# Kernel optimization log

Hardware: AMD Instinct MI355X
Metric: run time of the kernel (lower is better)

Reference implementation:

```python
import jax, jax.numpy as jnp
import numpy as np

SCALE = 1.0 / 8.0  # source divides sim_M by literal 8 (== sqrt(d_k=64))


def setup_inputs() -> dict:
    key = jax.random.key(0)
    ks = jax.random.split(key, 7)
    B, S, D = 16, 2048, 512  # D = n_head * d_k = 8 * 64
    s = 1.0 / np.sqrt(D)
    return {
        "x": jax.random.normal(ks[0], (B, S, D), dtype=jnp.float32),
        "Wq": jax.random.normal(ks[1], (D, D), dtype=jnp.float32) * s,
        "bq": jax.random.normal(ks[2], (D,), dtype=jnp.float32) * 0.01,
        "Wk": jax.random.normal(ks[3], (D, D), dtype=jnp.float32) * s,
        "bk": jax.random.normal(ks[4], (D,), dtype=jnp.float32) * 0.01,
        "Wv": jax.random.normal(ks[5], (D, D), dtype=jnp.float32) * s,
        "bv": jax.random.normal(ks[6], (D,), dtype=jnp.float32) * 0.01,
    }


def reference(x, Wq, bq, Wk, bk, Wv, bv):
    # Manual QKV projections (no head split, matching the source code)
    q = jnp.einsum("bsd,de->bse", x, Wq) + bq  # [B,S,D]
    k = jnp.einsum("bsd,de->bse", x, Wk) + bk  # [B,S,D]
    v = jnp.einsum("bsd,de->bse", x, Wv) + bv  # [B,S,D]
    # bmm -> softmax -> bmm attention
    sim = jnp.einsum("bqe,bke->bqk", q, k) * SCALE  # [B,S,S]
    attn = jax.nn.softmax(sim, axis=-1)
    out = jnp.einsum("bqk,bkd->bqd", attn, v)  # [B,S,D]
    return out
```

## Files before the change

kernel.cpp:

```cpp
#include <hip/hip_runtime.h>
#include <math.h>

typedef _Float16 f16;
typedef _Float16 f16x2 __attribute__((ext_vector_type(2)));
typedef _Float16 f16x8 __attribute__((ext_vector_type(8)));
typedef float f32x4 __attribute__((ext_vector_type(4)));

#define NB 16
#define SS 2048
#define DD 512

__device__ __forceinline__ void gl_lds16(const void* g, void* l) {
  __builtin_amdgcn_global_load_lds(
      (const __attribute__((address_space(1))) unsigned int*)g,
      (__attribute__((address_space(3))) unsigned int*)l, 16, 0, 0);
}

__device__ __forceinline__ int pk2(float a, float b) {
  f16x2 t = {(f16)a, (f16)b};
  return __builtin_bit_cast(int, t);
}

__global__ __launch_bounds__(256) void cast_kernel(const float* __restrict__ x,
                                                   f16* __restrict__ o) {
  size_t i = (size_t)blockIdx.x * 256 + threadIdx.x;
  const float4* p = (const float4*)x + i * 2;
  float4 a = p[0], b = p[1];
  f16x8 v = {(f16)a.x, (f16)a.y, (f16)a.z, (f16)a.w,
             (f16)b.x, (f16)b.y, (f16)b.z, (f16)b.w};
  *((f16x8*)o + i) = v;
}

__global__ __launch_bounds__(256) void transpose_kernel(
    const float* __restrict__ W0, const float* __restrict__ W1,
    const float* __restrict__ W2, f16* __restrict__ T0, f16* __restrict__ T1,
    f16* __restrict__ T2) {
  const float* W = (blockIdx.z == 0) ? W0 : (blockIdx.z == 1) ? W1 : W2;
  f16* Wt = (blockIdx.z == 0) ? T0 : (blockIdx.z == 1) ? T1 : T2;
  __shared__ float t[32][33];
  int bx = blockIdx.x * 32, by = blockIdx.y * 32;
  int c = threadIdx.x & 31, r0 = threadIdx.x >> 5;
  for (int r = r0; r < 32; r += 8) t[r][c] = W[(size_t)(by + r) * DD + bx + c];
  __syncthreads();
  for (int r = r0; r < 32; r += 8) Wt[(size_t)(bx + r) * DD + by + c] = (f16)t[c][r];
}

__global__ __launch_bounds__(512, 2) void gemmQKV_kernel(
    const f16* __restrict__ xh, const f16* __restrict__ WqT,
    const f16* __restrict__ WkT, const f16* __restrict__ WvT,
    f16* __restrict__ Qh, f16* __restrict__ Kh, f16* __restrict__ Vth,
    const float* __restrict__ bq, const float* __restrict__ bk,
    const float* __restrict__ bv) {
  const int wid = (blockIdx.x & 7) * 96 + (blockIdx.x >> 3);
  const f16* Wm;
  f16* C;
  const float* bias;
  size_t x0;
  size_t crow0, ccol0;
  int w0, ldc, bias_row;
  float scale;
  bool isV;
  if (wid < 512) {
    const bool isK = wid >= 256;
    const int r = wid & 255;
    x0 = (size_t)(r >> 1) * 256;
    w0 = (r & 1) * 256;
    Wm = isK ? WkT : WqT;
    C = isK ? Kh : Qh;
    bias = isK ? bk : bq;
    crow0 = x0;
    ccol0 = (size_t)w0;
    ldc = DD;
    bias_row = 0;
    scale = isK ? 1.0f : 0.125f;
    isV = false;
  } else {
    const int v = wid - 512;
    const int b = v >> 4, e = (v >> 3) & 1, s = v & 7;
    x0 = (size_t)b * SS + (size_t)s * 256;
    w0 = e * 256;
    Wm = WvT;
    C = Vth + (size_t)b * DD * SS;
    bias = bv;
    crow0 = (size_t)w0;
    ccol0 = (size_t)s * 256;
    ldc = SS;
    bias_row = 1;
    scale = 1.0f;
    isV = true;
  }
  __shared__ f16 Xsh[2][256][64];
  __shared__ f16 Wsh[2][256][64];
  const int tid = threadIdx.x, lane = tid & 63, wave = tid >> 6;
  const int wm2 = wave >> 2, wn2 = wave & 3;
  const int l15 = lane & 15, lq = lane >> 4;
  const int srow = lane >> 3;
  const int sseg = (lane & 7) ^ srow;
  f32x4 acc[8][4] = {};
  auto stage = [&](int sb, int kt) {
#pragma unroll
    for (int g = 0; g < 4; ++g) {
      const int r0 = wave * 32 + g * 8;
      gl_lds16(xh + (x0 + r0 + srow) * DD + kt * 64 + sseg * 8,
               (f16*)&Xsh[sb][r0][0] + lane * 8);
      gl_lds16(Wm + (size_t)(w0 + r0 + srow) * DD + kt * 64 + sseg * 8,
               (f16*)&Wsh[sb][r0][0] + lane * 8);
    }
  };
  stage(0, 0);
  asm volatile("s_waitcnt vmcnt(0)" ::: "memory");
  asm volatile("s_barrier" ::: "memory");
  for (int kt = 0; kt < 8; ++kt) {
    const int buf = kt & 1;
    if (kt < 7) stage(buf ^ 1, kt + 1);
    const f16(*As)[64] = isV ? Wsh[buf] : Xsh[buf];
    const f16(*Bs)[64] = isV ? Xsh[buf] : Wsh[buf];
#pragma unroll
    for (int ks = 0; ks < 2; ++ks) {
      const int seg = ((ks * 4 + lq) ^ (l15 & 7)) * 8;
      f16x8 bf[4];
#pragma unroll
      for (int j = 0; j < 4; ++j)
        bf[j] = *(const f16x8*)&Bs[64 * wn2 + 16 * j + l15][seg];
#pragma unroll
      for (int mh = 0; mh < 2; ++mh) {
        f16x8 af[4];
#pragma unroll
        for (int i = 0; i < 4; ++i)
          af[i] = *(const f16x8*)&As[128 * wm2 + 64 * mh + 16 * i + l15][seg];
        __builtin_amdgcn_s_setprio(1);
#pragma unroll
        for (int i = 0; i < 4; ++i)
#pragma unroll
          for (int j = 0; j < 4; ++j)
            acc[4 * mh + i][j] = __builtin_amdgcn_mfma_f32_16x16x32_f16(
                af[i], bf[j], acc[4 * mh + i][j], 0, 0, 0);
        __builtin_amdgcn_s_setprio(0);
        if (ks == 1 && mh == 1)
          asm volatile("s_waitcnt vmcnt(0)" ::: "memory");
        asm volatile("s_barrier" ::: "memory");
      }
    }
  }
#pragma unroll
  for (int i = 0; i < 8; ++i) {
    const int arow = 128 * wm2 + 16 * i + 4 * lq;
#pragma unroll
    for (int j = 0; j < 4; ++j) {
      const int acol = 64 * wn2 + 16 * j + l15;
#pragma unroll
      for (int r = 0; r < 4; ++r) {
        const size_t rr = crow0 + arow + r;
        const size_t cc = ccol0 + acol;
        const float bvv = bias_row ? bias[rr] : bias[cc];
        C[rr * ldc + cc] = (f16)((acc[i][j][r] + bvv) * scale);
      }
    }
  }
}

__global__ __launch_bounds__(512, 2) void attn_kernel(
    const f16* __restrict__ Q, const f16* __restrict__ K,
    const f16* __restrict__ Vt, float* __restrict__ out) {
  const int id = blockIdx.x;
  const int b = (id & 7) + ((id >> 7) << 3);
  const int qt = (id >> 3) & 15;
  const int tid = threadIdx.x, lane = tid & 63, wave = tid >> 6;
  const int l15 = lane & 15, lq = lane >> 4;

  __shared__ __align__(16) f16 Kl[2][32][520];
  __shared__ __align__(16) f16 Vl[2][512][32];

  const f16* qp = Q + ((size_t)(b * SS + qt * 128 + wave * 16 + l15)) * DD + lq * 8;
  f16x8 qf[16];
#pragma unroll
  for (int kk = 0; kk < 16; ++kk) qf[kk] = *(const f16x8*)(qp + kk * 32);

  const f16* Kb = K + (size_t)b * SS * DD;
  const f16* Vb = Vt + (size_t)b * DD * SS;

  const int sdata = (lane & 3) ^ ((lane >> 3) & 3);
  const int vrow = lane >> 2;
  const int vs_off = (lq ^ ((l15 >> 1) & 3)) * 8;

  f16x8 onef;
#pragma unroll
  for (int j = 0; j < 8; ++j) onef[j] = (f16)1.0f;

  auto stage = [&](int sb, int kb) {
#pragma unroll
    for (int rr = 0; rr < 4; ++rr) {
      int row = wave * 4 + rr;
      gl_lds16(Kb + ((size_t)(kb + row)) * DD + lane * 8, &Kl[sb][row][lane * 8]);
    }
#pragma unroll
    for (int i = 0; i < 4; ++i) {
      int e0 = wave * 64 + i * 16;
      gl_lds16(Vb + (size_t)(e0 + vrow) * SS + kb + sdata * 8,
               (f16*)&Vl[sb][e0][0] + lane * 8);
    }
  };

  stage(0, 0);
  __syncthreads();

  f32x4 acco[32] = {};
  f32x4 accl = {};
  float m = -1e30f;

  for (int it = 0; it < 64; ++it) {
    const int buf = it & 1;
    if (it < 63) stage(buf ^ 1, (it + 1) * 32);
    f32x4 sa0 = {}, sa1 = {};
#pragma unroll
    for (int kk = 0; kk < 16; ++kk) {
      f16x8 b0 = *(const f16x8*)&Kl[buf][l15][kk * 32 + lq * 8];
      f16x8 b1 = *(const f16x8*)&Kl[buf][16 + l15][kk * 32 + lq * 8];
      sa0 = __builtin_amdgcn_mfma_f32_16x16x32_f16(b0, qf[kk], sa0, 0, 0, 0);
      sa1 = __builtin_amdgcn_mfma_f32_16x16x32_f16(b1, qf[kk], sa1, 0, 0, 0);
    }
    float lm = fmaxf(fmaxf(fmaxf(sa0[0], sa0[1]), fmaxf(sa0[2], sa0[3])),
                     fmaxf(fmaxf(sa1[0], sa1[1]), fmaxf(sa1[2], sa1[3])));
    if (__any(lm > m + 8.0f)) {
      float mx = lm;
      mx = fmaxf(mx, __shfl_xor(mx, 16));
      mx = fmaxf(mx, __shfl_xor(mx, 32));
      float mn = fmaxf(m, mx);
      float al = __expf(m - mn);
      m = mn;
      float alr[4];
#pragma unroll
      for (int r = 0; r < 4; ++r) alr[r] = __shfl(al, 4 * lq + r);
#pragma unroll
      for (int t = 0; t < 32; ++t)
#pragma unroll
        for (int r = 0; r < 4; ++r) acco[t][r] *= alr[r];
#pragma unroll
      for (int r = 0; r < 4; ++r) accl[r] *= alr[r];
    }
    int A0 = pk2(__expf(sa0[0] - m), __expf(sa0[1] - m));
    int A1 = pk2(__expf(sa0[2] - m), __expf(sa0[3] - m));
    int B0 = pk2(__expf(sa1[0] - m), __expf(sa1[1] - m));
    int B1 = pk2(__expf(sa1[2] - m), __expf(sa1[3] - m));
    const bool low = (lq < 2);
    int s0 = low ? B0 : A0, s1 = low ? B1 : A1;
    int X0 = __shfl_xor(s0, 32), X1 = __shfl_xor(s1, 32);
    int Y0 = low ? A0 : B0, Y1 = low ? A1 : B1;
    const bool sx = (lq == 0) || (lq == 3);
    int t0 = sx ? X0 : Y0, t1 = sx ? X1 : Y1;
    int Z0 = __shfl_xor(t0, 16), Z1 = __shfl_xor(t1, 16);
    union PU { int i[4]; f16x8 v; } pu;
    pu.i[0] = (lq == 0) ? Y0 : ((lq == 2) ? X0 : Z0);
    pu.i[1] = (lq == 0) ? Y1 : ((lq == 2) ? X1 : Z1);
    pu.i[2] = (lq == 1) ? X0 : ((lq == 3) ? Y0 : Z0);
    pu.i[3] = (lq == 1) ? X1 : ((lq == 3) ? Y1 : Z1);
    f16x8 pa = pu.v;
    accl = __builtin_amdgcn_mfma_f32_16x16x32_f16(pa, onef, accl, 0, 0, 0);
#pragma unroll
    for (int nn = 0; nn < 32; ++nn) {
      f16x8 vf = *(const f16x8*)&Vl[buf][nn * 16 + l15][vs_off];
      acco[nn] = __builtin_amdgcn_mfma_f32_16x16x32_f16(pa, vf, acco[nn], 0, 0, 0);
    }
    __syncthreads();
  }
  float inv[4];
#pragma unroll
  for (int r = 0; r < 4; ++r) inv[r] = 1.0f / accl[r];
  const size_t ob = ((size_t)(b * SS + qt * 128 + wave * 16 + 4 * lq)) * DD + l15;
#pragma unroll
  for (int nn = 0; nn < 32; ++nn)
#pragma unroll
    for (int r = 0; r < 4; ++r)
      out[ob + (size_t)r * DD + nn * 16] = acco[nn][r] * inv[r];
}

extern "C" void kernel_launch(void* const* d_in, const int* in_sizes, int n_in,
                              void* d_out, int out_size, void* d_ws, size_t ws_size,
                              hipStream_t stream) {
  const float* x = (const float*)d_in[0];
  const float* Wq = (const float*)d_in[1];
  const float* bq = (const float*)d_in[2];
  const float* Wk = (const float*)d_in[3];
  const float* bk = (const float*)d_in[4];
  const float* Wv = (const float*)d_in[5];
  const float* bv = (const float*)d_in[6];
  float* out = (float*)d_out;
  f16* ws = (f16*)d_ws;
  const size_t NX = (size_t)NB * SS * DD;
  f16* xh = ws;
  f16* Qh = ws + NX;
  f16* Kh = ws + 2 * NX;
  f16* Vth = ws + 3 * NX;
  f16* WqT = ws + 4 * NX;
  f16* WkT = WqT + DD * DD;
  f16* WvT = WkT + DD * DD;

  cast_kernel<<<NX / 8 / 256, 256, 0, stream>>>(x, xh);
  transpose_kernel<<<dim3(16, 16, 3), 256, 0, stream>>>(Wq, Wk, Wv, WqT, WkT, WvT);
  gemmQKV_kernel<<<768, 512, 0, stream>>>(xh, WqT, WkT, WvT, Qh, Kh, Vth, bq, bk, bv);
  attn_kernel<<<256, 512, 0, stream>>>(Qh, Kh, Vth, out);
}
```

Baseline: 365.1 us.

## Process two 16-row query tiles per wave in attention, halving waves per block

Each wave in the attention kernel now handles 32 query rows (two 16-row tiles) instead of 16, with 4 waves per block instead of 8. Each K and V fragment read from LDS is reused across two MFMA chains, which halves LDS read traffic per flop. In exchange every wave holds twice the accumulators and Q fragments, which raises register pressure (launch bounds become 256,1). It also leaves fewer waves per CU to hide latency.

```diff
diff --git a/kernel.cpp b/kernel.cpp
--- a/kernel.cpp
+++ b/kernel.cpp
@@ -159,7 +159,7 @@
   }
 }
 
-__global__ __launch_bounds__(512, 2) void attn_kernel(
+__global__ __launch_bounds__(256, 1) void attn_kernel(
     const f16* __restrict__ Q, const f16* __restrict__ K,
     const f16* __restrict__ Vt, float* __restrict__ out) {
   const int id = blockIdx.x;
@@ -171,10 +171,12 @@
   __shared__ __align__(16) f16 Kl[2][32][520];
   __shared__ __align__(16) f16 Vl[2][512][32];
 
-  const f16* qp = Q + ((size_t)(b * SS + qt * 128 + wave * 16 + l15)) * DD + lq * 8;
-  f16x8 qf[16];
-#pragma unroll
-  for (int kk = 0; kk < 16; ++kk) qf[kk] = *(const f16x8*)(qp + kk * 32);
+  const f16* qp0 = Q + ((size_t)(b * SS + qt * 128 + wave * 32 + l15)) * DD + lq * 8;
+  f16x8 qf0[16], qf1[16];
+#pragma unroll
+  for (int kk = 0; kk < 16; ++kk) qf0[kk] = *(const f16x8*)(qp0 + kk * 32);
+#pragma unroll
+  for (int kk = 0; kk < 16; ++kk) qf1[kk] = *(const f16x8*)(qp0 + 16 * DD + kk * 32);
 
   const f16* Kb = K + (size_t)b * SS * DD;
   const f16* Vb = Vt + (size_t)b * DD * SS;
@@ -189,13 +191,13 @@
 
   auto stage = [&](int sb, int kb) {
 #pragma unroll
-    for (int rr = 0; rr < 4; ++rr) {
-      int row = wave * 4 + rr;
+    for (int rr = 0; rr < 8; ++rr) {
+      int row = wave * 8 + rr;
       gl_lds16(Kb + ((size_t)(kb + row)) * DD + lane * 8, &Kl[sb][row][lane * 8]);
     }
 #pragma unroll
-    for (int i = 0; i < 4; ++i) {
-      int e0 = wave * 64 + i * 16;
+    for (int i = 0; i < 8; ++i) {
+      int e0 = wave * 128 + i * 16;
       gl_lds16(Vb + (size_t)(e0 + vrow) * SS + kb + sdata * 8,
                (f16*)&Vl[sb][e0][0] + lane * 8);
     }
@@ -204,74 +206,90 @@
   stage(0, 0);
   __syncthreads();
 
-  f32x4 acco[32] = {};
-  f32x4 accl = {};
-  float m = -1e30f;
+  f32x4 acco0[32] = {}, acco1[32] = {};
+  f32x4 accl0 = {}, accl1 = {};
+  float m0 = -1e30f, m1 = -1e30f;
 
   for (int it = 0; it < 64; ++it) {
     const int buf = it & 1;
     if (it < 63) stage(buf ^ 1, (it + 1) * 32);
-    f32x4 sa0 = {}, sa1 = {};
+    f32x4 s00 = {}, s01 = {}, s10 = {}, s11 = {};
 #pragma unroll
     for (int kk = 0; kk < 16; ++kk) {
       f16x8 b0 = *(const f16x8*)&Kl[buf][l15][kk * 32 + lq * 8];
       f16x8 b1 = *(const f16x8*)&Kl[buf][16 + l15][kk * 32 + lq * 8];
-      sa0 = __builtin_amdgcn_mfma_f32_16x16x32_f16(b0, qf[kk], sa0, 0, 0, 0);
-      sa1 = __builtin_amdgcn_mfma_f32_16x16x32_f16(b1, qf[kk], sa1, 0, 0, 0);
-    }
-    float lm = fmaxf(fmaxf(fmaxf(sa0[0], sa0[1]), fmaxf(sa0[2], sa0[3])),
-                     fmaxf(fmaxf(sa1[0], sa1[1]), fmaxf(sa1[2], sa1[3])));
-    if (__any(lm > m + 8.0f)) {
-      float mx = lm;
-      mx = fmaxf(mx, __shfl_xor(mx, 16));
-      mx = fmaxf(mx, __shfl_xor(mx, 32));
-      float mn = fmaxf(m, mx);
-      float al = __expf(m - mn);
-      m = mn;
-      float alr[4];
-#pragma unroll
-      for (int r = 0; r < 4; ++r) alr[r] = __shfl(al, 4 * lq + r);
-#pragma unroll
-      for (int t = 0; t < 32; ++t)
-#pragma unroll
-        for (int r = 0; r < 4; ++r) acco[t][r] *= alr[r];
-#pragma unroll
-      for (int r = 0; r < 4; ++r) accl[r] *= alr[r];
-    }
-    int A0 = pk2(__expf(sa0[0] - m), __expf(sa0[1] - m));
-    int A1 = pk2(__expf(sa0[2] - m), __expf(sa0[3] - m));
-    int B0 = pk2(__expf(sa1[0] - m), __expf(sa1[1] - m));
-    int B1 = pk2(__expf(sa1[2] - m), __expf(sa1[3] - m));
-    const bool low = (lq < 2);
-    int s0 = low ? B0 : A0, s1 = low ? B1 : A1;
-    int X0 = __shfl_xor(s0, 32), X1 = __shfl_xor(s1, 32);
-    int Y0 = low ? A0 : B0, Y1 = low ? A1 : B1;
-    const bool sx = (lq == 0) || (lq == 3);
-    int t0 = sx ? X0 : Y0, t1 = sx ? X1 : Y1;
-    int Z0 = __shfl_xor(t0, 16), Z1 = __shfl_xor(t1, 16);
-    union PU { int i[4]; f16x8 v; } pu;
-    pu.i[0] = (lq == 0) ? Y0 : ((lq == 2) ? X0 : Z0);
-    pu.i[1] = (lq == 0) ? Y1 : ((lq == 2) ? X1 : Z1);
-    pu.i[2] = (lq == 1) ? X0 : ((lq == 3) ? Y0 : Z0);
-    pu.i[3] = (lq == 1) ? X1 : ((lq == 3) ? Y1 : Z1);
-    f16x8 pa = pu.v;
-    accl = __builtin_amdgcn_mfma_f32_16x16x32_f16(pa, onef, accl, 0, 0, 0);
+      s00 = __builtin_amdgcn_mfma_f32_16x16x32_f16(b0, qf0[kk], s00, 0, 0, 0);
+      s01 = __builtin_amdgcn_mfma_f32_16x16x32_f16(b1, qf0[kk], s01, 0, 0, 0);
+      s10 = __builtin_amdgcn_mfma_f32_16x16x32_f16(b0, qf1[kk], s10, 0, 0, 0);
+      s11 = __builtin_amdgcn_mfma_f32_16x16x32_f16(b1, qf1[kk], s11, 0, 0, 0);
+    }
+    f16x8 pa0, pa1;
+#pragma unroll
+    for (int h = 0; h < 2; ++h) {
+      f32x4 sa0 = h ? s10 : s00;
+      f32x4 sa1 = h ? s11 : s01;
+      float& m = h ? m1 : m0;
+      f32x4& accl = h ? accl1 : accl0;
+      f32x4* acco = h ? acco1 : acco0;
+      float lm = fmaxf(fmaxf(fmaxf(sa0[0], sa0[1]), fmaxf(sa0[2], sa0[3])),
+                       fmaxf(fmaxf(sa1[0], sa1[1]), fmaxf(sa1[2], sa1[3])));
+      if (__any(lm > m + 8.0f)) {
+        float mx = fmaxf(lm, __shfl_xor(lm, 16));
+        mx = fmaxf(mx, __shfl_xor(mx, 32));
+        float mn = fmaxf(m, mx);
+        float al = __expf(m - mn);
+        m = mn;
+        float alr[4];
+#pragma unroll
+        for (int r = 0; r < 4; ++r) alr[r] = __shfl(al, 4 * lq + r);
+#pragma unroll
+        for (int t = 0; t < 32; ++t)
+#pragma unroll
+          for (int r = 0; r < 4; ++r) acco[t][r] *= alr[r];
+#pragma unroll
+        for (int r = 0; r < 4; ++r) accl[r] *= alr[r];
+      }
+      int A0 = pk2(__expf(sa0[0] - m), __expf(sa0[1] - m));
+      int A1 = pk2(__expf(sa0[2] - m), __expf(sa0[3] - m));
+      int B0 = pk2(__expf(sa1[0] - m), __expf(sa1[1] - m));
+      int B1 = pk2(__expf(sa1[2] - m), __expf(sa1[3] - m));
+      const bool low = (lq < 2);
+      int t0s = low ? B0 : A0, t1s = low ? B1 : A1;
+      int X0 = __shfl_xor(t0s, 32), X1 = __shfl_xor(t1s, 32);
+      int Y0 = low ? A0 : B0, Y1 = low ? A1 : B1;
+      const bool sx = (lq == 0) || (lq == 3);
+      int u0 = sx ? X0 : Y0, u1 = sx ? X1 : Y1;
+      int Z0 = __shfl_xor(u0, 16), Z1 = __shfl_xor(u1, 16);
+      union PU { int i[4]; f16x8 v; } pu;
+      pu.i[0] = (lq == 0) ? Y0 : ((lq == 2) ? X0 : Z0);
+      pu.i[1] = (lq == 0) ? Y1 : ((lq == 2) ? X1 : Z1);
+      pu.i[2] = (lq == 1) ? X0 : ((lq == 3) ? Y0 : Z0);
+      pu.i[3] = (lq == 1) ? X1 : ((lq == 3) ? Y1 : Z1);
+      f16x8 pa = pu.v;
+      accl = __builtin_amdgcn_mfma_f32_16x16x32_f16(pa, onef, accl, 0, 0, 0);
+      if (h) pa1 = pa; else pa0 = pa;
+    }
 #pragma unroll
     for (int nn = 0; nn < 32; ++nn) {
       f16x8 vf = *(const f16x8*)&Vl[buf][nn * 16 + l15][vs_off];
-      acco[nn] = __builtin_amdgcn_mfma_f32_16x16x32_f16(pa, vf, acco[nn], 0, 0, 0);
+      acco0[nn] = __builtin_amdgcn_mfma_f32_16x16x32_f16(pa0, vf, acco0[nn], 0, 0, 0);
+      acco1[nn] = __builtin_amdgcn_mfma_f32_16x16x32_f16(pa1, vf, acco1[nn], 0, 0, 0);
     }
     __syncthreads();
   }
-  float inv[4];
-#pragma unroll
-  for (int r = 0; r < 4; ++r) inv[r] = 1.0f / accl[r];
-  const size_t ob = ((size_t)(b * SS + qt * 128 + wave * 16 + 4 * lq)) * DD + l15;
+  float inv0[4], inv1[4];
+#pragma unroll
+  for (int r = 0; r < 4; ++r) inv0[r] = 1.0f / accl0[r];
+#pragma unroll
+  for (int r = 0; r < 4; ++r) inv1[r] = 1.0f / accl1[r];
+  const size_t ob = ((size_t)(b * SS + qt * 128 + wave * 32 + 4 * lq)) * DD + l15;
 #pragma unroll
   for (int nn = 0; nn < 32; ++nn)
 #pragma unroll
-    for (int r = 0; r < 4; ++r)
-      out[ob + (size_t)r * DD + nn * 16] = acco[nn][r] * inv[r];
+    for (int r = 0; r < 4; ++r) {
+      out[ob + (size_t)r * DD + nn * 16] = acco0[nn][r] * inv0[r];
+      out[ob + (size_t)(16 + r) * DD + nn * 16] = acco1[nn][r] * inv1[r];
+    }
 }
 
 extern "C" void kernel_launch(void* const* d_in, const int* in_sizes, int n_in,
@@ -298,5 +316,5 @@
   cast_kernel<<<NX / 8 / 256, 256, 0, stream>>>(x, xh);
   transpose_kernel<<<dim3(16, 16, 3), 256, 0, stream>>>(Wq, Wk, Wv, WqT, WkT, WvT);
   gemmQKV_kernel<<<768, 512, 0, stream>>>(xh, WqT, WkT, WvT, Qh, Kh, Vth, bq, bk, bv);
-  attn_kernel<<<256, 512, 0, stream>>>(Qh, Kh, Vth, out);
-}
+  attn_kernel<<<256, 256, 0, stream>>>(Qh, Kh, Vth, out);
+}
```

New measurement: 1.207 ms. 3.3x slower.
